# Optimization experiments

Hardware: AMD Instinct MI355X
Metric: run time of the kernel (lower is better)

Reference implementation:

```python
import jax, jax.numpy as jnp
import numpy as np

LN_EPS = 1e-5
BN_EPS = 1e-5
HEADS = 8
KERNEL = 31
GROUP_SIZE = 8  # depthwise_conv groups = inner_dim // 8


def _ln(x, g, b):
    mu = jnp.mean(x, axis=-1, keepdims=True)
    var = jnp.var(x, axis=-1, keepdims=True)
    return (x - mu) * jax.lax.rsqrt(var + LN_EPS) * g + b


def _ff(x, g, b, w_in, b_in, w_out, b_out):
    h = _ln(x, g, b)
    y = h @ w_in.T + b_in
    a, c = jnp.split(y, 2, axis=-1)
    return (jax.nn.silu(a) * c) @ w_out.T + b_out


def _attn(x, g, b, wqkv, bqkv, wo, bo):
    B, S, _ = x.shape
    h = _ln(x, g, b)
    qkv = (h @ wqkv.T + bqkv).reshape(B, S, 3, HEADS, -1).transpose(2, 0, 3, 1, 4)
    q, k, v = qkv[0], qkv[1], qkv[2]  # [B,H,S,D]
    scale = q.shape[-1] ** -0.5
    scores = jnp.einsum('bhqd,bhkd->bhqk', q, k) * scale
    w = jax.nn.softmax(scores, axis=-1)
    o = jnp.einsum('bhqk,bhkd->bhqd', w, v)
    o = o.transpose(0, 2, 1, 3).reshape(B, S, -1)
    return o @ wo.T + bo


def _conv(x, g, b, pw1_w, pw1_b, dw_w, dw_b, bn_g, bn_b, bn_m, bn_v, pw2_w, pw2_b):
    h = _ln(x, g, b).transpose(0, 2, 1)  # [B, C, S]
    y = jnp.einsum('oc,bcs->bos', pw1_w[:, :, 0], h) + pw1_b[:, None]
    a, c = jnp.split(y, 2, axis=1)
    y = a * jax.nn.sigmoid(c)  # GLU over channel dim -> [B, inner, S]
    pad = (KERNEL - 1) // 2
    groups = y.shape[1] // dw_w.shape[1]  # inner_dim // 8
    y = jax.lax.conv_general_dilated(
        y, dw_w, window_strides=(1,), padding=[(pad, pad)],
        dimension_numbers=('NCH', 'OIH', 'NCH'), feature_group_count=groups)
    y = y + dw_b[:, None]
    y = (y - bn_m[:, None]) * jax.lax.rsqrt(bn_v[:, None] + BN_EPS) * bn_g[:, None] + bn_b[:, None]
    y = jax.nn.silu(y)
    y = jnp.einsum('oc,bcs->bos', pw2_w[:, :, 0], y) + pw2_b[:, None]
    return y.transpose(0, 2, 1)


def setup_inputs() -> dict:
    key = jax.random.key(0)
    dim, mult, exp = 512, 4, 2
    inner = dim * exp  # 1024
    ks = jax.random.split(key, 16)
    n = lambda k, shp: (jax.random.normal(k, shp, dtype=jnp.float32) * 0.02)
    d = {}
    d['x'] = jax.random.normal(ks[0], (8, 1024, dim), dtype=jnp.float32)
    # ff1
    d['ff1_g'] = jnp.ones((dim,), jnp.float32); d['ff1_b'] = jnp.zeros((dim,), jnp.float32)
    d['ff1_win'] = n(ks[1], (dim * mult * 2, dim)); d['ff1_bin'] = jnp.zeros((dim * mult * 2,), jnp.float32)
    d['ff1_wout'] = n(ks[2], (dim, dim * mult)); d['ff1_bout'] = jnp.zeros((dim,), jnp.float32)
    # attn
    d['attn_g'] = jnp.ones((dim,), jnp.float32); d['attn_b'] = jnp.zeros((dim,), jnp.float32)
    d['wqkv'] = n(ks[3], (3 * dim, dim)); d['bqkv'] = jnp.zeros((3 * dim,), jnp.float32)
    d['wo'] = n(ks[4], (dim, dim)); d['bo'] = jnp.zeros((dim,), jnp.float32)
    # conv
    d['conv_g'] = jnp.ones((dim,), jnp.float32); d['conv_b'] = jnp.zeros((dim,), jnp.float32)
    d['pw1_w'] = n(ks[5], (inner * 2, dim, 1)); d['pw1_b'] = jnp.zeros((inner * 2,), jnp.float32)
    d['dw_w'] = n(ks[6], (inner, GROUP_SIZE, KERNEL)); d['dw_b'] = jnp.zeros((inner,), jnp.float32)
    d['bn_g'] = jnp.ones((inner,), jnp.float32); d['bn_b'] = jnp.zeros((inner,), jnp.float32)
    d['bn_m'] = jnp.zeros((inner,), jnp.float32); d['bn_v'] = jnp.ones((inner,), jnp.float32)
    d['pw2_w'] = n(ks[7], (dim, inner, 1)); d['pw2_b'] = jnp.zeros((dim,), jnp.float32)
    # ff2
    d['ff2_g'] = jnp.ones((dim,), jnp.float32); d['ff2_b'] = jnp.zeros((dim,), jnp.float32)
    d['ff2_win'] = n(ks[8], (dim * mult * 2, dim)); d['ff2_bin'] = jnp.zeros((dim * mult * 2,), jnp.float32)
    d['ff2_wout'] = n(ks[9], (dim, dim * mult)); d['ff2_bout'] = jnp.zeros((dim,), jnp.float32)
    # final norm
    d['fn_g'] = jnp.ones((dim,), jnp.float32); d['fn_b'] = jnp.zeros((dim,), jnp.float32)
    return d


def reference(x, ff1_g, ff1_b, ff1_win, ff1_bin, ff1_wout, ff1_bout,
              attn_g, attn_b, wqkv, bqkv, wo, bo,
              conv_g, conv_b, pw1_w, pw1_b, dw_w, dw_b, bn_g, bn_b, bn_m, bn_v, pw2_w, pw2_b,
              ff2_g, ff2_b, ff2_win, ff2_bin, ff2_wout, ff2_bout, fn_g, fn_b):
    x = x + 0.5 * _ff(x, ff1_g, ff1_b, ff1_win, ff1_bin, ff1_wout, ff1_bout)
    x = x + _attn(x, attn_g, attn_b, wqkv, bqkv, wo, bo)
    x = x + _conv(x, conv_g, conv_b, pw1_w, pw1_b, dw_w, dw_b, bn_g, bn_b, bn_m, bn_v, pw2_w, pw2_b)
    x = x + 0.5 * _ff(x, ff2_g, ff2_b, ff2_win, ff2_bin, ff2_wout, ff2_bout)
    return _ln(x, fn_g, fn_b)
```

## Files before the change

kernel.cpp:

```cpp
#include <hip/hip_runtime.h>

#define SEQ   1024
#define BATCH 8
#define DIM   512
#define NTOK  (SEQ * BATCH)

typedef unsigned short ushort_t;
typedef unsigned int uint_t;
typedef __attribute__((ext_vector_type(8))) short s16x8;
typedef __attribute__((ext_vector_type(4))) float f32x4;

union F4 { float4 v; float f[4]; };

__device__ __forceinline__ float sigmoid_f(float x) { return 1.0f / (1.0f + expf(-x)); }
__device__ __forceinline__ float silu_f(float x)    { return x * sigmoid_f(x); }

__device__ __forceinline__ ushort_t f2bf(float x) {
  uint_t u = __float_as_uint(x);
  return (ushort_t)((u + 0x7FFFu + ((u >> 16) & 1u)) >> 16);
}
__device__ __forceinline__ float bf2f(ushort_t h) {
  return __uint_as_float(((uint_t)h) << 16);
}

__device__ __forceinline__ void gload16(const void* g, void* l) {
  __builtin_amdgcn_global_load_lds(
      (const __attribute__((address_space(1))) void*)g,
      (__attribute__((address_space(3))) void*)l,
      16, 0, 0);
}

__global__ __launch_bounds__(256) void f2b_kernel(
    const float* __restrict__ in, ushort_t* __restrict__ out, int n8)
{
  const int i = blockIdx.x * 256 + threadIdx.x;
  if (i >= n8) return;
  F4 x0, x1;
  x0.v = *(const float4*)(in + (size_t)i * 8);
  x1.v = *(const float4*)(in + (size_t)i * 8 + 4);
  uint4 o;
  o.x = (uint_t)f2bf(x0.f[0]) | ((uint_t)f2bf(x0.f[1]) << 16);
  o.y = (uint_t)f2bf(x0.f[2]) | ((uint_t)f2bf(x0.f[3]) << 16);
  o.z = (uint_t)f2bf(x1.f[0]) | ((uint_t)f2bf(x1.f[1]) << 16);
  o.w = (uint_t)f2bf(x1.f[2]) | ((uint_t)f2bf(x1.f[3]) << 16);
  *(uint4*)(out + (size_t)i * 8) = o;
}

template <int BF>
__global__ __launch_bounds__(256) void ln512_kernel(
    const float* __restrict__ in, const float* __restrict__ g,
    const float* __restrict__ b, void* __restrict__ outv)
{
  const int row = blockIdx.x;
  const int t   = threadIdx.x;
  const float2 v = ((const float2*)(in + (size_t)row * DIM))[t];
  float sum = v.x + v.y;
  float sq  = v.x * v.x + v.y * v.y;
  #pragma unroll
  for (int m = 32; m >= 1; m >>= 1) {
    sum += __shfl_xor(sum, m, 64);
    sq  += __shfl_xor(sq,  m, 64);
  }
  __shared__ float s1[4], s2[4];
  if ((t & 63) == 0) { s1[t >> 6] = sum; s2[t >> 6] = sq; }
  __syncthreads();
  const float tot = s1[0] + s1[1] + s1[2] + s1[3];
  const float tsq = s2[0] + s2[1] + s2[2] + s2[3];
  const float mu   = tot * (1.0f / DIM);
  const float var  = tsq * (1.0f / DIM) - mu * mu;
  const float rinv = rsqrtf(var + 1e-5f);
  const float2 gv = ((const float2*)g)[t];
  const float2 bv = ((const float2*)b)[t];
  float2 o;
  o.x = (v.x - mu) * rinv * gv.x + bv.x;
  o.y = (v.y - mu) * rinv * gv.y + bv.y;
  if (BF) {
    ((uint_t*)outv)[(size_t)row * 256 + t] =
        (uint_t)f2bf(o.x) | ((uint_t)f2bf(o.y) << 16);
  } else {
    ((float2*)outv)[(size_t)row * 256 + t] = o;
  }
}

template <int EPI>
__global__ __launch_bounds__(256) void gemm_bf16(
    const ushort_t* __restrict__ A, const ushort_t* __restrict__ W,
    const float* __restrict__ bias, float* __restrict__ out,
    int N, int K, const float* __restrict__ res, float alpha)
{
  __shared__ ushort_t As[128 * 32];
  __shared__ ushort_t Ws[128 * 32];
  const int t    = threadIdx.x;
  const int lane = t & 63;
  const int w    = t >> 6;
  const int wm   = w >> 1, wn = w & 1;
  const int m0   = blockIdx.y << 7, n0 = blockIdx.x << 7;

  f32x4 acc[4][4] = {};

  const int lds0 = __builtin_amdgcn_readfirstlane((w * 64) * 16);
  const int lds1 = __builtin_amdgcn_readfirstlane((256 + w * 64) * 16);
  const int r0c  = t >> 2;
  const int r1c  = 64 + (t >> 2);
  const int cc   = (t & 3) << 3;

  for (int k0 = 0; k0 < K; k0 += 32) {
    gload16(A + (size_t)(m0 + r0c) * K + k0 + cc, (char*)As + lds0);
    gload16(A + (size_t)(m0 + r1c) * K + k0 + cc, (char*)As + lds1);
    gload16(W + (size_t)(n0 + r0c) * K + k0 + cc, (char*)Ws + lds0);
    gload16(W + (size_t)(n0 + r1c) * K + k0 + cc, (char*)Ws + lds1);
    __syncthreads();
    s16x8 a[4], b[4];
    #pragma unroll
    for (int i = 0; i < 4; ++i)
      a[i] = *(const s16x8*)&As[(wm * 64 + i * 16 + (lane & 15)) * 32 + ((lane >> 4) << 3)];
    #pragma unroll
    for (int j = 0; j < 4; ++j)
      b[j] = *(const s16x8*)&Ws[(wn * 64 + j * 16 + (lane & 15)) * 32 + ((lane >> 4) << 3)];
    #pragma unroll
    for (int i = 0; i < 4; ++i)
      #pragma unroll
      for (int j = 0; j < 4; ++j)
        acc[i][j] = __builtin_amdgcn_mfma_f32_16x16x32_bf16(a[i], b[j], acc[i][j], 0, 0, 0);
    __syncthreads();
  }

  #pragma unroll
  for (int i = 0; i < 4; ++i) {
    #pragma unroll
    for (int j = 0; j < 4; ++j) {
      const int col  = n0 + wn * 64 + j * 16 + (lane & 15);
      const int rowb = m0 + wm * 64 + i * 16 + ((lane >> 4) << 2);
      const float bc = bias[col];
      #pragma unroll
      for (int r = 0; r < 4; ++r) {
        const size_t idx = (size_t)(rowb + r) * N + col;
        float v = acc[i][j][r] + bc;
        if (EPI == 1) v = res[idx] + alpha * v;
        out[idx] = v;
      }
    }
  }
}

__global__ __launch_bounds__(256) void gemm_qkv_bf16(
    const ushort_t* __restrict__ A, const ushort_t* __restrict__ W,
    const float* __restrict__ bias, ushort_t* __restrict__ qkvb,
    ushort_t* __restrict__ Vt, int K)
{
  const int N = 1536;
  __shared__ ushort_t As[128 * 32];
  __shared__ ushort_t Ws[128 * 32];
  const int t    = threadIdx.x;
  const int lane = t & 63;
  const int w    = t >> 6;
  const int wm   = w >> 1, wn = w & 1;
  const int m0   = blockIdx.y << 7, n0 = blockIdx.x << 7;

  f32x4 acc[4][4] = {};

  const int lds0 = __builtin_amdgcn_readfirstlane((w * 64) * 16);
  const int lds1 = __builtin_amdgcn_readfirstlane((256 + w * 64) * 16);
  const int r0c  = t >> 2;
  const int r1c  = 64 + (t >> 2);
  const int cc   = (t & 3) << 3;

  for (int k0 = 0; k0 < K; k0 += 32) {
    gload16(A + (size_t)(m0 + r0c) * K + k0 + cc, (char*)As + lds0);
    gload16(A + (size_t)(m0 + r1c) * K + k0 + cc, (char*)As + lds1);
    gload16(W + (size_t)(n0 + r0c) * K + k0 + cc, (char*)Ws + lds0);
    gload16(W + (size_t)(n0 + r1c) * K + k0 + cc, (char*)Ws + lds1);
    __syncthreads();
    s16x8 a[4], b[4];
    #pragma unroll
    for (int i = 0; i < 4; ++i)
      a[i] = *(const s16x8*)&As[(wm * 64 + i * 16 + (lane & 15)) * 32 + ((lane >> 4) << 3)];
    #pragma unroll
    for (int j = 0; j < 4; ++j)
      b[j] = *(const s16x8*)&Ws[(wn * 64 + j * 16 + (lane & 15)) * 32 + ((lane >> 4) << 3)];
    #pragma unroll
    for (int i = 0; i < 4; ++i)
      #pragma unroll
      for (int j = 0; j < 4; ++j)
        acc[i][j] = __builtin_amdgcn_mfma_f32_16x16x32_bf16(a[i], b[j], acc[i][j], 0, 0, 0);
    __syncthreads();
  }

  #pragma unroll
  for (int i = 0; i < 4; ++i) {
    #pragma unroll
    for (int j = 0; j < 4; ++j) {
      const int col  = n0 + wn * 64 + j * 16 + (lane & 15);
      const int rowb = m0 + wm * 64 + i * 16 + ((lane >> 4) << 2);
      const float bc = bias[col];
      if (col < 1024) {
        #pragma unroll
        for (int r = 0; r < 4; ++r)
          qkvb[(size_t)(rowb + r) * N + col] = f2bf(acc[i][j][r] + bc);
      } else {
        const int vc = col - 1024;
        const int hh = vc >> 6, d = vc & 63;
        const int bb = rowb >> 10, s = rowb & 1023;
        ushort4 o;
        o.x = f2bf(acc[i][j][0] + bc);
        o.y = f2bf(acc[i][j][1] + bc);
        o.z = f2bf(acc[i][j][2] + bc);
        o.w = f2bf(acc[i][j][3] + bc);
        *(ushort4*)&Vt[(size_t)((bb * 8 + hh) * 64 + d) * 1024 + s] = o;
      }
    }
  }
}

template <int CGLU>
__global__ __launch_bounds__(256) void gemm_glu_bf16(
    const ushort_t* __restrict__ A, const ushort_t* __restrict__ W,
    const float* __restrict__ bias, ushort_t* __restrict__ out,
    int NG, int K)
{
  __shared__ ushort_t As[128 * 32];
  __shared__ ushort_t Was[64 * 32];
  __shared__ ushort_t Wcs[64 * 32];
  const int t    = threadIdx.x;
  const int lane = t & 63;
  const int w    = t >> 6;
  const int wm   = w >> 1, wn = w & 1;
  const int m0   = blockIdx.y << 7, n0 = blockIdx.x << 6;

  f32x4 acca[4][2] = {};
  f32x4 accc[4][2] = {};

  const int lds0 = __builtin_amdgcn_readfirstlane((w * 64) * 16);
  const int lds1 = __builtin_amdgcn_readfirstlane((256 + w * 64) * 16);
  const int r0c  = t >> 2;
  const int r1c  = 64 + (t >> 2);
  const int cc   = (t & 3) << 3;

  const ushort_t* Wc = W + (size_t)NG * K;

  for (int k0 = 0; k0 < K; k0 += 32) {
    gload16(A  + (size_t)(m0 + r0c) * K + k0 + cc, (char*)As  + lds0);
    gload16(A  + (size_t)(m0 + r1c) * K + k0 + cc, (char*)As  + lds1);
    gload16(W  + (size_t)(n0 + r0c) * K + k0 + cc, (char*)Was + lds0);
    gload16(Wc + (size_t)(n0 + r0c) * K + k0 + cc, (char*)Wcs + lds0);
    __syncthreads();
    s16x8 a[4], ba[2], bc[2];
    #pragma unroll
    for (int i = 0; i < 4; ++i)
      a[i] = *(const s16x8*)&As[(wm * 64 + i * 16 + (lane & 15)) * 32 + ((lane >> 4) << 3)];
    #pragma unroll
    for (int j = 0; j < 2; ++j) {
      const int roff = (wn * 32 + j * 16 + (lane & 15)) * 32 + ((lane >> 4) << 3);
      ba[j] = *(const s16x8*)&Was[roff];
      bc[j] = *(const s16x8*)&Wcs[roff];
    }
    #pragma unroll
    for (int i = 0; i < 4; ++i)
      #pragma unroll
      for (int j = 0; j < 2; ++j) {
        acca[i][j] = __builtin_amdgcn_mfma_f32_16x16x32_bf16(a[i], ba[j], acca[i][j], 0, 0, 0);
        accc[i][j] = __builtin_amdgcn_mfma_f32_16x16x32_bf16(a[i], bc[j], accc[i][j], 0, 0, 0);
      }
    __syncthreads();
  }

  #pragma unroll
  for (int i = 0; i < 4; ++i) {
    #pragma unroll
    for (int j = 0; j < 2; ++j) {
      const int col  = n0 + wn * 32 + j * 16 + (lane & 15);
      const int rowb = m0 + wm * 64 + i * 16 + ((lane >> 4) << 2);
      const float b1 = bias[col];
      const float b2 = bias[NG + col];
      #pragma unroll
      for (int r = 0; r < 4; ++r) {
        const float av = acca[i][j][r] + b1;
        const float cv = accc[i][j][r] + b2;
        const float o  = CGLU ? (av * sigmoid_f(cv)) : (silu_f(av) * cv);
        out[(size_t)(rowb + r) * NG + col] = f2bf(o);
      }
    }
  }
}

__global__ __launch_bounds__(256) void attn_mfma(
    const ushort_t* __restrict__ qkv, const ushort_t* __restrict__ Vt,
    ushort_t* __restrict__ out)
{
  __shared__ ushort_t Ks[64 * 64];
  __shared__ ushort_t Vs[64 * 64];
  __shared__ ushort_t Ps[4][16 * 64];

  const int t    = threadIdx.x;
  const int lane = t & 63;
  const int w    = t >> 6;
  const int i    = lane & 15;
  const int g    = lane >> 4;
  const int bh   = blockIdx.x;
  const int b    = bh >> 3, h = bh & 7;
  const int qt   = blockIdx.y;

  s16x8 qf[2];
  {
    const ushort_t* qrow = qkv + (size_t)(b * SEQ + qt * 64 + w * 16 + i) * 1536 + h * 64;
    qf[0] = *(const s16x8*)(qrow + g * 8);
    qf[1] = *(const s16x8*)(qrow + 32 + g * 8);
  }

  float m_[4], l_[4];
  f32x4 po[4] = {};
  #pragma unroll
  for (int r = 0; r < 4; ++r) { m_[r] = -1e30f; l_[r] = 0.0f; }

  const int e0   = w * 2;
  const int off0 = __builtin_amdgcn_readfirstlane(e0 * 1024);
  const int off1 = __builtin_amdgcn_readfirstlane(e0 * 1024 + 1024);

  for (int kvt = 0; kvt < 16; ++kvt) {
    __syncthreads();
    {
      const int s_a = e0 * 64 + lane;
      const int ra = s_a >> 3, ca = (s_a & 7) ^ (ra & 7);
      const int s_b = s_a + 64;
      const int rb = s_b >> 3, cb2 = (s_b & 7) ^ (rb & 7);
      gload16(qkv + (size_t)(b * SEQ + kvt * 64 + ra) * 1536 + 512 + h * 64 + ca * 8,
              (char*)Ks + off0);
      gload16(qkv + (size_t)(b * SEQ + kvt * 64 + rb) * 1536 + 512 + h * 64 + cb2 * 8,
              (char*)Ks + off1);
      gload16(Vt + (size_t)(bh * 64 + ra) * SEQ + kvt * 64 + ca * 8,
              (char*)Vs + off0);
      gload16(Vt + (size_t)(bh * 64 + rb) * SEQ + kvt * 64 + cb2 * 8,
              (char*)Vs + off1);
    }
    __syncthreads();

    f32x4 sc[4] = {};
    #pragma unroll
    for (int jj = 0; jj < 4; ++jj) {
      const int row = jj * 16 + i;
      #pragma unroll
      for (int dd = 0; dd < 2; ++dd) {
        const int byteoff = row * 128 + ((dd * 64 + g * 16) ^ ((row & 7) << 4));
        const s16x8 kf = *(const s16x8*)((const char*)Ks + byteoff);
        sc[jj] = __builtin_amdgcn_mfma_f32_16x16x32_bf16(qf[dd], kf, sc[jj], 0, 0, 0);
      }
    }

    #pragma unroll
    for (int r = 0; r < 4; ++r) {
      float v0 = sc[0][r] * 0.125f, v1 = sc[1][r] * 0.125f;
      float v2 = sc[2][r] * 0.125f, v3 = sc[3][r] * 0.125f;
      float mx = fmaxf(fmaxf(v0, v1), fmaxf(v2, v3));
      mx = fmaxf(mx, __shfl_xor(mx, 1));
      mx = fmaxf(mx, __shfl_xor(mx, 2));
      mx = fmaxf(mx, __shfl_xor(mx, 4));
      mx = fmaxf(mx, __shfl_xor(mx, 8));
      const float mn = fmaxf(m_[r], mx);
      const float al = __expf(m_[r] - mn);
      const float p0 = __expf(v0 - mn), p1 = __expf(v1 - mn);
      const float p2 = __expf(v2 - mn), p3 = __expf(v3 - mn);
      float rs = p0 + p1 + p2 + p3;
      rs += __shfl_xor(rs, 1); rs += __shfl_xor(rs, 2);
      rs += __shfl_xor(rs, 4); rs += __shfl_xor(rs, 8);
      l_[r] = l_[r] * al + rs;
      m_[r] = mn;
      #pragma unroll
      for (int dt = 0; dt < 4; ++dt) po[dt][r] *= al;
      const int q = 4 * g + r;
      const int key = (q & 7) << 4;
      ushort_t* pb = &Ps[w][0];
      ((ushort_t*)((char*)pb + q * 128 + ((2 * i) ^ key)))[0]       = f2bf(p0);
      ((ushort_t*)((char*)pb + q * 128 + ((32 + 2 * i) ^ key)))[0]  = f2bf(p1);
      ((ushort_t*)((char*)pb + q * 128 + ((64 + 2 * i) ^ key)))[0]  = f2bf(p2);
      ((ushort_t*)((char*)pb + q * 128 + ((96 + 2 * i) ^ key)))[0]  = f2bf(p3);
    }

    #pragma unroll
    for (int kc = 0; kc < 2; ++kc) {
      const int pbyte = i * 128 + ((kc * 64 + g * 16) ^ ((i & 7) << 4));
      const s16x8 pf = *(const s16x8*)((const char*)&Ps[w][0] + pbyte);
      #pragma unroll
      for (int dt = 0; dt < 4; ++dt) {
        const int vrow = dt * 16 + i;
        const int vbyte = vrow * 128 + ((kc * 64 + g * 16) ^ ((vrow & 7) << 4));
        const s16x8 vf = *(const s16x8*)((const char*)Vs + vbyte);
        po[dt] = __builtin_amdgcn_mfma_f32_16x16x32_bf16(pf, vf, po[dt], 0, 0, 0);
      }
    }
  }

  #pragma unroll
  for (int r = 0; r < 4; ++r) {
    const float inv = 1.0f / l_[r];
    const size_t row = (size_t)(b * SEQ + qt * 64 + w * 16 + 4 * g + r);
    #pragma unroll
    for (int dt = 0; dt < 4; ++dt)
      out[row * 512 + h * 64 + dt * 16 + i] = f2bf(po[dt][r] * inv);
  }
}

__global__ __launch_bounds__(256) void dwconv_kernel(
    const ushort_t* __restrict__ in, const float* __restrict__ w,
    const float* __restrict__ dwb, const float* __restrict__ bng,
    const float* __restrict__ bnb, const float* __restrict__ bnm,
    const float* __restrict__ bnv, ushort_t* __restrict__ out)
{
  __shared__ __align__(16) float tile[94][64];
  const int s0 = blockIdx.x << 6;
  const int c0 = blockIdx.y << 6;
  const int b  = blockIdx.z;
  const int t  = threadIdx.x;

  {
    const int cl4 = (t & 15) << 2;
    #pragma unroll
    for (int it = 0; it < 6; ++it) {
      const int rr = it * 16 + (t >> 4);
      if (rr < 94) {
        const int gs = s0 - 15 + rr;
        float4 fv = make_float4(0.f, 0.f, 0.f, 0.f);
        if (gs >= 0 && gs < SEQ) {
          ushort4 uv = *(const ushort4*)(in + (size_t)(b * SEQ + gs) * 1024 + c0 + cl4);
          fv = make_float4(bf2f(uv.x), bf2f(uv.y), bf2f(uv.z), bf2f(uv.w));
        }
        *(float4*)&tile[rr][cl4] = fv;
      }
    }
  }
  __syncthreads();

  const int c  = t & 63;
  const int sb = (t >> 6) << 4;
  const int gc = c0 + c;

  float acc[16] = {};
  const float* wc = w + (size_t)gc * 248;
  for (int ci = 0; ci < 8; ++ci) {
    const int cl = (c & 56) | ci;
    float v[46];
    #pragma unroll
    for (int r = 0; r < 46; ++r) v[r] = tile[sb + r][cl];
    #pragma unroll
    for (int tap = 0; tap < 31; ++tap) {
      const float wv = wc[ci * 31 + tap];
      #pragma unroll
      for (int j = 0; j < 16; ++j) acc[j] = fmaf(wv, v[j + tap], acc[j]);
    }
  }

  const float bias = dwb[gc];
  const float mean = bnm[gc];
  const float rstd = rsqrtf(bnv[gc] + 1e-5f);
  const float gg   = bng[gc];
  const float bb2  = bnb[gc];
  #pragma unroll
  for (int j = 0; j < 16; ++j) {
    const int s = s0 + sb + j;
    float y = acc[j] + bias;
    y = (y - mean) * rstd * gg + bb2;
    out[(size_t)(b * SEQ + s) * 1024 + gc] = f2bf(silu_f(y));
  }
}

extern "C" void kernel_launch(void* const* d_in, const int* in_sizes, int n_in,
                              void* d_out, int out_size, void* d_ws, size_t ws_size,
                              hipStream_t stream)
{
  (void)in_sizes; (void)n_in; (void)out_size; (void)ws_size;
  const float* x        = (const float*)d_in[0];
  const float* ff1_g    = (const float*)d_in[1];
  const float* ff1_b    = (const float*)d_in[2];
  const float* ff1_win  = (const float*)d_in[3];
  const float* ff1_bin  = (const float*)d_in[4];
  const float* ff1_wout = (const float*)d_in[5];
  const float* ff1_bout = (const float*)d_in[6];
  const float* attn_g   = (const float*)d_in[7];
  const float* attn_b   = (const float*)d_in[8];
  const float* wqkv     = (const float*)d_in[9];
  const float* bqkv     = (const float*)d_in[10];
  const float* wo       = (const float*)d_in[11];
  const float* bo       = (const float*)d_in[12];
  const float* conv_g   = (const float*)d_in[13];
  const float* conv_b   = (const float*)d_in[14];
  const float* pw1_w    = (const float*)d_in[15];
  const float* pw1_b    = (const float*)d_in[16];
  const float* dw_w     = (const float*)d_in[17];
  const float* dw_b     = (const float*)d_in[18];
  const float* bn_g     = (const float*)d_in[19];
  const float* bn_b     = (const float*)d_in[20];
  const float* bn_m     = (const float*)d_in[21];
  const float* bn_v     = (const float*)d_in[22];
  const float* pw2_w    = (const float*)d_in[23];
  const float* pw2_b    = (const float*)d_in[24];
  const float* ff2_g    = (const float*)d_in[25];
  const float* ff2_b    = (const float*)d_in[26];
  const float* ff2_win  = (const float*)d_in[27];
  const float* ff2_bin  = (const float*)d_in[28];
  const float* ff2_wout = (const float*)d_in[29];
  const float* ff2_bout = (const float*)d_in[30];
  const float* fn_g     = (const float*)d_in[31];
  const float* fn_b     = (const float*)d_in[32];

  char* wsb = (char*)d_ws;
  float*    xc    = (float*)(wsb);
  ushort_t* qkvb  = (ushort_t*)(wsb + (size_t)(16 << 20));
  ushort_t* vtb   = (ushort_t*)(wsb + (size_t)(40 << 20));
  ushort_t* h_bf  = (ushort_t*)(wsb + (size_t)(48 << 20));
  ushort_t* g_bf  = (ushort_t*)(wsb + (size_t)(56 << 20));
  ushort_t* tb_bf = (ushort_t*)(wsb + (size_t)(88 << 20));
  ushort_t* cv_bf = (ushort_t*)(wsb + (size_t)(96 << 20));
  ushort_t* wb    = (ushort_t*)(wsb + (size_t)(112 << 20));

  ushort_t* ff1win_b  = wb;
  ushort_t* ff1wout_b = ff1win_b + 4096 * 512;
  ushort_t* wqkv_b    = ff1wout_b + 512 * 2048;
  ushort_t* wo_b      = wqkv_b + 1536 * 512;
  ushort_t* pw1w_b    = wo_b + 512 * 512;
  ushort_t* pw2w_b    = pw1w_b + 2048 * 512;
  ushort_t* ff2win_b  = pw2w_b + 512 * 1024;
  ushort_t* ff2wout_b = ff2win_b + 4096 * 512;

  float* outp = (float*)d_out;
  const dim3 B256(256);

  struct Cvt { const float* s; ushort_t* d; int n; };
  const Cvt cv[8] = {
      {ff1_win,  ff1win_b,  4096 * 512}, {ff1_wout, ff1wout_b, 512 * 2048},
      {wqkv,     wqkv_b,    1536 * 512}, {wo,       wo_b,      512 * 512},
      {pw1_w,    pw1w_b,    2048 * 512}, {pw2_w,    pw2w_b,    512 * 1024},
      {ff2_win,  ff2win_b,  4096 * 512}, {ff2_wout, ff2wout_b, 512 * 2048}};
  for (int i = 0; i < 8; ++i) {
    const int n8 = cv[i].n / 8;
    f2b_kernel<<<dim3((n8 + 255) / 256), B256, 0, stream>>>(cv[i].s, cv[i].d, n8);
  }

  ln512_kernel<1><<<dim3(NTOK), B256, 0, stream>>>(x, ff1_g, ff1_b, h_bf);
  gemm_glu_bf16<0><<<dim3(32, 64), B256, 0, stream>>>(h_bf, ff1win_b, ff1_bin, g_bf, 2048, 512);
  gemm_bf16<1><<<dim3(4, 64), B256, 0, stream>>>(g_bf, ff1wout_b, ff1_bout, xc, 512, 2048, x, 0.5f);

  ln512_kernel<1><<<dim3(NTOK), B256, 0, stream>>>(xc, attn_g, attn_b, h_bf);
  gemm_qkv_bf16<<<dim3(12, 64), B256, 0, stream>>>(h_bf, wqkv_b, bqkv, qkvb, vtb, 512);
  attn_mfma<<<dim3(64, 16), B256, 0, stream>>>(qkvb, vtb, tb_bf);
  gemm_bf16<1><<<dim3(4, 64), B256, 0, stream>>>(tb_bf, wo_b, bo, xc, 512, 512, xc, 1.0f);

  ln512_kernel<1><<<dim3(NTOK), B256, 0, stream>>>(xc, conv_g, conv_b, h_bf);
  gemm_glu_bf16<1><<<dim3(16, 64), B256, 0, stream>>>(h_bf, pw1w_b, pw1_b, g_bf, 1024, 512);
  dwconv_kernel<<<dim3(16, 16, 8), B256, 0, stream>>>(g_bf, dw_w, dw_b, bn_g, bn_b, bn_m, bn_v, cv_bf);
  gemm_bf16<1><<<dim3(4, 64), B256, 0, stream>>>(cv_bf, pw2w_b, pw2_b, xc, 512, 1024, xc, 1.0f);

  ln512_kernel<1><<<dim3(NTOK), B256, 0, stream>>>(xc, ff2_g, ff2_b, h_bf);
  gemm_glu_bf16<0><<<dim3(32, 64), B256, 0, stream>>>(h_bf, ff2win_b, ff2_bin, g_bf, 2048, 512);
  gemm_bf16<1><<<dim3(4, 64), B256, 0, stream>>>(g_bf, ff2wout_b, ff2_bout, xc, 512, 2048, xc, 0.5f);

  ln512_kernel<0><<<dim3(NTOK), B256, 0, stream>>>(xc, fn_g, fn_b, outp);
}
```

Measured before the change: 622.9 us.

## Batch weight casts, use one wave per LayerNorm row, restructure depthwise conv

The eight fp32→bf16 weight-cast launches are merged into one kernel that finds its source tensor from cumulative offsets. LayerNorm now gives each 512-wide row to one wavefront, using float4 loads and a shuffle-only reduction with no shared memory or block barrier. The depthwise conv maps lanes to sequence positions and loops over 8-channel groups, so weights load as wave-uniform scalar loads. It uses a padded LDS tile to avoid bank conflicts and stages outputs through LDS for coalesced 16-byte bf16 stores. The trade-offs are a per-element search in the cast kernel and more LDS passes and barriers in the conv.

```diff
diff --git a/kernel.cpp b/kernel.cpp
--- a/kernel.cpp
+++ b/kernel.cpp
@@ -30,20 +30,30 @@
       16, 0, 0);
 }
 
-__global__ __launch_bounds__(256) void f2b_kernel(
-    const float* __restrict__ in, ushort_t* __restrict__ out, int n8)
+struct CastArgs {
+  const float* src[8];
+  ushort_t*    dst[8];
+  int          cum8[8];
+};
+
+__global__ __launch_bounds__(256) void f2b_multi(CastArgs a, int total8)
 {
   const int i = blockIdx.x * 256 + threadIdx.x;
-  if (i >= n8) return;
+  if (i >= total8) return;
+  int s = 0;
+  #pragma unroll
+  for (int k = 1; k < 8; ++k) s += (i >= a.cum8[k]) ? 1 : 0;
+  const int j = i - a.cum8[s];
+  const float* src = a.src[s] + (size_t)j * 8;
   F4 x0, x1;
-  x0.v = *(const float4*)(in + (size_t)i * 8);
-  x1.v = *(const float4*)(in + (size_t)i * 8 + 4);
+  x0.v = *(const float4*)(src);
+  x1.v = *(const float4*)(src + 4);
   uint4 o;
   o.x = (uint_t)f2bf(x0.f[0]) | ((uint_t)f2bf(x0.f[1]) << 16);
   o.y = (uint_t)f2bf(x0.f[2]) | ((uint_t)f2bf(x0.f[3]) << 16);
   o.z = (uint_t)f2bf(x1.f[0]) | ((uint_t)f2bf(x1.f[1]) << 16);
   o.w = (uint_t)f2bf(x1.f[2]) | ((uint_t)f2bf(x1.f[3]) << 16);
-  *(uint4*)(out + (size_t)i * 8) = o;
+  *(uint4*)(a.dst[s] + (size_t)j * 8) = o;
 }
 
 template <int BF>
@@ -51,34 +61,46 @@
     const float* __restrict__ in, const float* __restrict__ g,
     const float* __restrict__ b, void* __restrict__ outv)
 {
-  const int row = blockIdx.x;
-  const int t   = threadIdx.x;
-  const float2 v = ((const float2*)(in + (size_t)row * DIM))[t];
-  float sum = v.x + v.y;
-  float sq  = v.x * v.x + v.y * v.y;
+  const int row = blockIdx.x * 4 + (threadIdx.x >> 6);
+  const int l   = threadIdx.x & 63;
+  const float* rp = in + (size_t)row * DIM + l * 8;
+  F4 v0, v1;
+  v0.v = *(const float4*)(rp);
+  v1.v = *(const float4*)(rp + 4);
+  float sum = 0.f, sq = 0.f;
+  #pragma unroll
+  for (int j = 0; j < 4; ++j) { sum += v0.f[j] + v1.f[j];
+                                sq  += v0.f[j]*v0.f[j] + v1.f[j]*v1.f[j]; }
   #pragma unroll
   for (int m = 32; m >= 1; m >>= 1) {
     sum += __shfl_xor(sum, m, 64);
     sq  += __shfl_xor(sq,  m, 64);
   }
-  __shared__ float s1[4], s2[4];
-  if ((t & 63) == 0) { s1[t >> 6] = sum; s2[t >> 6] = sq; }
-  __syncthreads();
-  const float tot = s1[0] + s1[1] + s1[2] + s1[3];
-  const float tsq = s2[0] + s2[1] + s2[2] + s2[3];
-  const float mu   = tot * (1.0f / DIM);
-  const float var  = tsq * (1.0f / DIM) - mu * mu;
+  const float mu   = sum * (1.0f / DIM);
+  const float var  = sq * (1.0f / DIM) - mu * mu;
   const float rinv = rsqrtf(var + 1e-5f);
-  const float2 gv = ((const float2*)g)[t];
-  const float2 bv = ((const float2*)b)[t];
-  float2 o;
-  o.x = (v.x - mu) * rinv * gv.x + bv.x;
-  o.y = (v.y - mu) * rinv * gv.y + bv.y;
+  F4 g0, g1, b0, b1;
+  g0.v = *(const float4*)(g + l * 8);     g1.v = *(const float4*)(g + l * 8 + 4);
+  b0.v = *(const float4*)(b + l * 8);     b1.v = *(const float4*)(b + l * 8 + 4);
+  float o[8];
+  #pragma unroll
+  for (int j = 0; j < 4; ++j) {
+    o[j]     = (v0.f[j] - mu) * rinv * g0.f[j] + b0.f[j];
+    o[4 + j] = (v1.f[j] - mu) * rinv * g1.f[j] + b1.f[j];
+  }
   if (BF) {
-    ((uint_t*)outv)[(size_t)row * 256 + t] =
-        (uint_t)f2bf(o.x) | ((uint_t)f2bf(o.y) << 16);
+    uint4 u;
+    u.x = (uint_t)f2bf(o[0]) | ((uint_t)f2bf(o[1]) << 16);
+    u.y = (uint_t)f2bf(o[2]) | ((uint_t)f2bf(o[3]) << 16);
+    u.z = (uint_t)f2bf(o[4]) | ((uint_t)f2bf(o[5]) << 16);
+    u.w = (uint_t)f2bf(o[6]) | ((uint_t)f2bf(o[7]) << 16);
+    *(uint4*)((ushort_t*)outv + (size_t)row * DIM + l * 8) = u;
   } else {
-    ((float2*)outv)[(size_t)row * 256 + t] = o;
+    F4 w0, w1;
+    #pragma unroll
+    for (int j = 0; j < 4; ++j) { w0.f[j] = o[j]; w1.f[j] = o[4 + j]; }
+    *(float4*)((float*)outv + (size_t)row * DIM + l * 8)     = w0.v;
+    *(float4*)((float*)outv + (size_t)row * DIM + l * 8 + 4) = w1.v;
   }
 }
 
@@ -405,7 +427,7 @@
     const float* __restrict__ bnb, const float* __restrict__ bnm,
     const float* __restrict__ bnv, ushort_t* __restrict__ out)
 {
-  __shared__ __align__(16) float tile[94][64];
+  __shared__ float tile[94][65];
   const int s0 = blockIdx.x << 6;
   const int c0 = blockIdx.y << 6;
   const int b  = blockIdx.z;
@@ -423,42 +445,71 @@
           ushort4 uv = *(const ushort4*)(in + (size_t)(b * SEQ + gs) * 1024 + c0 + cl4);
           fv = make_float4(bf2f(uv.x), bf2f(uv.y), bf2f(uv.z), bf2f(uv.w));
         }
-        *(float4*)&tile[rr][cl4] = fv;
+        tile[rr][cl4 + 0] = fv.x;
+        tile[rr][cl4 + 1] = fv.y;
+        tile[rr][cl4 + 2] = fv.z;
+        tile[rr][cl4 + 3] = fv.w;
       }
     }
   }
   __syncthreads();
 
-  const int c  = t & 63;
-  const int sb = (t >> 6) << 4;
-  const int gc = c0 + c;
-
-  float acc[16] = {};
-  const float* wc = w + (size_t)gc * 248;
-  for (int ci = 0; ci < 8; ++ci) {
-    const int cl = (c & 56) | ci;
-    float v[46];
-    #pragma unroll
-    for (int r = 0; r < 46; ++r) v[r] = tile[sb + r][cl];
-    #pragma unroll
-    for (int tap = 0; tap < 31; ++tap) {
-      const float wv = wc[ci * 31 + tap];
-      #pragma unroll
-      for (int j = 0; j < 16; ++j) acc[j] = fmaf(wv, v[j + tap], acc[j]);
-    }
-  }
-
-  const float bias = dwb[gc];
-  const float mean = bnm[gc];
-  const float rstd = rsqrtf(bnv[gc] + 1e-5f);
-  const float gg   = bng[gc];
-  const float bb2  = bnb[gc];
-  #pragma unroll
-  for (int j = 0; j < 16; ++j) {
-    const int s = s0 + sb + j;
-    float y = acc[j] + bias;
-    y = (y - mean) * rstd * gg + bb2;
-    out[(size_t)(b * SEQ + s) * 1024 + gc] = f2bf(silu_f(y));
+  const int wv   = t >> 6;
+  const int lane = t & 63;
+
+  float res[16];
+  #pragma unroll
+  for (int grp = 0; grp < 2; ++grp) {
+    const int chb = wv * 16 + grp * 8;
+    const int gcb = __builtin_amdgcn_readfirstlane(c0 + chb);
+    const float* wbase = w + (size_t)gcb * 248;
+    float acc[8] = {};
+    for (int ci = 0; ci < 8; ++ci) {
+      float win[31];
+      #pragma unroll
+      for (int r = 0; r < 31; ++r) win[r] = tile[lane + r][chb + ci];
+      const float* wp = wbase + ci * 31;
+      #pragma unroll
+      for (int co = 0; co < 8; ++co) {
+        #pragma unroll
+        for (int tap = 0; tap < 31; ++tap)
+          acc[co] = fmaf(wp[co * 248 + tap], win[tap], acc[co]);
+      }
+    }
+    #pragma unroll
+    for (int co = 0; co < 8; ++co) res[grp * 8 + co] = acc[co];
+  }
+
+  __syncthreads();
+  #pragma unroll
+  for (int grp = 0; grp < 2; ++grp) {
+    const int chb = wv * 16 + grp * 8;
+    const int gcb = __builtin_amdgcn_readfirstlane(c0 + chb);
+    #pragma unroll
+    for (int co = 0; co < 8; ++co) {
+      const int gc = gcb + co;
+      float y = res[grp * 8 + co] + dwb[gc];
+      y = (y - bnm[gc]) * rsqrtf(bnv[gc] + 1e-5f) * bng[gc] + bnb[gc];
+      tile[lane][chb + co] = silu_f(y);
+    }
+  }
+  __syncthreads();
+  {
+    const int r  = t >> 2;
+    const int cq = (t & 3) << 4;
+    uint4 o1;
+    uint_t p[8];
+    #pragma unroll
+    for (int j = 0; j < 8; ++j) {
+      const float a = tile[r][cq + 2 * j];
+      const float c = tile[r][cq + 2 * j + 1];
+      p[j] = (uint_t)f2bf(a) | ((uint_t)f2bf(c) << 16);
+    }
+    ushort_t* dst = out + (size_t)(b * SEQ + s0 + r) * 1024 + c0 + cq;
+    o1 = make_uint4(p[0], p[1], p[2], p[3]);
+    *(uint4*)dst = o1;
+    o1 = make_uint4(p[4], p[5], p[6], p[7]);
+    *(uint4*)(dst + 8) = o1;
   }
 }
 
@@ -523,34 +574,36 @@
   float* outp = (float*)d_out;
   const dim3 B256(256);
 
-  struct Cvt { const float* s; ushort_t* d; int n; };
-  const Cvt cv[8] = {
-      {ff1_win,  ff1win_b,  4096 * 512}, {ff1_wout, ff1wout_b, 512 * 2048},
-      {wqkv,     wqkv_b,    1536 * 512}, {wo,       wo_b,      512 * 512},
-      {pw1_w,    pw1w_b,    2048 * 512}, {pw2_w,    pw2w_b,    512 * 1024},
-      {ff2_win,  ff2win_b,  4096 * 512}, {ff2_wout, ff2wout_b, 512 * 2048}};
-  for (int i = 0; i < 8; ++i) {
-    const int n8 = cv[i].n / 8;
-    f2b_kernel<<<dim3((n8 + 255) / 256), B256, 0, stream>>>(cv[i].s, cv[i].d, n8);
-  }
-
-  ln512_kernel<1><<<dim3(NTOK), B256, 0, stream>>>(x, ff1_g, ff1_b, h_bf);
+  {
+    CastArgs a;
+    const float* srcs[8] = {ff1_win, ff1_wout, wqkv, wo, pw1_w, pw2_w, ff2_win, ff2_wout};
+    ushort_t*    dsts[8] = {ff1win_b, ff1wout_b, wqkv_b, wo_b, pw1w_b, pw2w_b, ff2win_b, ff2wout_b};
+    const int    ns[8]   = {4096*512, 512*2048, 1536*512, 512*512,
+                            2048*512, 512*1024, 4096*512, 512*2048};
+    int cum = 0;
+    for (int i = 0; i < 8; ++i) {
+      a.src[i] = srcs[i]; a.dst[i] = dsts[i]; a.cum8[i] = cum; cum += ns[i] / 8;
+    }
+    f2b_multi<<<dim3((cum + 255) / 256), B256, 0, stream>>>(a, cum);
+  }
+
+  ln512_kernel<1><<<dim3(NTOK / 4), B256, 0, stream>>>(x, ff1_g, ff1_b, h_bf);
   gemm_glu_bf16<0><<<dim3(32, 64), B256, 0, stream>>>(h_bf, ff1win_b, ff1_bin, g_bf, 2048, 512);
   gemm_bf16<1><<<dim3(4, 64), B256, 0, stream>>>(g_bf, ff1wout_b, ff1_bout, xc, 512, 2048, x, 0.5f);
 
-  ln512_kernel<1><<<dim3(NTOK), B256, 0, stream>>>(xc, attn_g, attn_b, h_bf);
+  ln512_kernel<1><<<dim3(NTOK / 4), B256, 0, stream>>>(xc, attn_g, attn_b, h_bf);
   gemm_qkv_bf16<<<dim3(12, 64), B256, 0, stream>>>(h_bf, wqkv_b, bqkv, qkvb, vtb, 512);
   attn_mfma<<<dim3(64, 16), B256, 0, stream>>>(qkvb, vtb, tb_bf);
   gemm_bf16<1><<<dim3(4, 64), B256, 0, stream>>>(tb_bf, wo_b, bo, xc, 512, 512, xc, 1.0f);
 
-  ln512_kernel<1><<<dim3(NTOK), B256, 0, stream>>>(xc, conv_g, conv_b, h_bf);
+  ln512_kernel<1><<<dim3(NTOK / 4), B256, 0, stream>>>(xc, conv_g, conv_b, h_bf);
   gemm_glu_bf16<1><<<dim3(16, 64), B256, 0, stream>>>(h_bf, pw1w_b, pw1_b, g_bf, 1024, 512);
   dwconv_kernel<<<dim3(16, 16, 8), B256, 0, stream>>>(g_bf, dw_w, dw_b, bn_g, bn_b, bn_m, bn_v, cv_bf);
   gemm_bf16<1><<<dim3(4, 64), B256, 0, stream>>>(cv_bf, pw2w_b, pw2_b, xc, 512, 1024, xc, 1.0f);
 
-  ln512_kernel<1><<<dim3(NTOK), B256, 0, stream>>>(xc, ff2_g, ff2_b, h_bf);
+  ln512_kernel<1><<<dim3(NTOK / 4), B256, 0, stream>>>(xc, ff2_g, ff2_b, h_bf);
   gemm_glu_bf16<0><<<dim3(32, 64), B256, 0, stream>>>(h_bf, ff2win_b, ff2_bin, g_bf, 2048, 512);
   gemm_bf16<1><<<dim3(4, 64), B256, 0, stream>>>(g_bf, ff2wout_b, ff2_bout, xc, 512, 2048, xc, 0.5f);
 
-  ln512_kernel<0><<<dim3(NTOK), B256, 0, stream>>>(xc, fn_g, fn_b, outp);
-}
+  ln512_kernel<0><<<dim3(NTOK / 4), B256, 0, stream>>>(xc, fn_g, fn_b, outp);
+}
```

Result: slower. 671.2 us (+7.7%).
